# Kernel optimization log

Hardware: AMD Instinct MI355X
Metric: run time of the kernel (lower is better)

Reference implementation:

```python
import jax, jax.numpy as jnp
import numpy as np

B, T, V, E, H = 512, 256, 50000, 512, 1024


def setup_inputs() -> dict:
    key = jax.random.key(0)
    ks = jax.random.split(key, 10)
    s_in = 1.0 / np.sqrt(E + H)  # torch Linear default init scale
    s_fc = 1.0 / np.sqrt(H)
    return {
        "x": jax.random.randint(ks[0], (B, T), 0, V),
        "emb": jax.random.normal(ks[1], (V, E), dtype=jnp.float32),
        "W_r": jax.random.uniform(ks[2], (E + H, H), jnp.float32, -s_in, s_in),
        "b_r": jax.random.uniform(ks[3], (H,), jnp.float32, -s_in, s_in),
        "W_z": jax.random.uniform(ks[4], (E + H, H), jnp.float32, -s_in, s_in),
        "b_z": jax.random.uniform(ks[5], (H,), jnp.float32, -s_in, s_in),
        "W_c": jax.random.uniform(ks[6], (E + H, H), jnp.float32, -s_in, s_in),
        "b_c": jax.random.uniform(ks[7], (H,), jnp.float32, -s_in, s_in),
        "W_fc": jax.random.uniform(ks[8], (H, 1), jnp.float32, -s_fc, s_fc),
        "b_fc": jax.random.uniform(ks[9], (1,), jnp.float32, -s_fc, s_fc),
    }


def reference(x, emb, W_r, b_r, W_z, b_z, W_c, b_c, W_fc, b_fc):
    embedded = emb[x]                      # [B, T, E]
    xs = jnp.swapaxes(embedded, 0, 1)      # [T, B, E] for scan over time
    h0 = jnp.zeros((x.shape[0], H), dtype=emb.dtype)

    # fuse r and z gates: same input, one GEMM
    W_rz = jnp.concatenate([W_r, W_z], axis=1)   # [E+H, 2H]
    b_rz = jnp.concatenate([b_r, b_z], axis=0)   # [2H]

    def step(h, xt):
        combined = jnp.concatenate([xt, h], axis=1)          # [B, E+H]
        rz = jax.nn.sigmoid(combined @ W_rz + b_rz)          # [B, 2H]
        r, z = rz[:, :H], rz[:, H:]
        cc = jnp.concatenate([xt, r * h], axis=1)            # [B, E+H]
        h_tilde = jnp.tanh(cc @ W_c + b_c)                   # [B, H]
        h_new = (1.0 - z) * h + z * h_tilde
        return h_new, None

    h_T, _ = jax.lax.scan(step, h0, xs)
    return jax.nn.sigmoid(h_T @ W_fc + b_fc)                 # [B, 1]
```

## Files before the change

kernel.cpp:

```cpp
#include <hip/hip_runtime.h>
#include <hip/hip_bf16.h>

#define B_ 512
#define T_ 256
#define E_ 512
#define H_ 1024
#define K_ 1536

typedef __attribute__((ext_vector_type(4))) float f32x4;
typedef __attribute__((ext_vector_type(8))) short s16x8;
typedef __attribute__((ext_vector_type(4))) unsigned int u32x4;
typedef __attribute__((ext_vector_type(2))) unsigned int u32x2;

typedef unsigned int u32_g __attribute__((address_space(1)));
typedef unsigned int u32_l __attribute__((address_space(3)));

static __device__ __forceinline__ void gload16(const void* g, void* l) {
    __builtin_amdgcn_global_load_lds((const u32_g*)g, (u32_l*)l, 16, 0, 0);
}

static __device__ __forceinline__ short f2b(float f) {
    union { float f; unsigned u; } v; v.f = f;
    unsigned r = v.u + 0x7FFFu + ((v.u >> 16) & 1u);
    return (short)(r >> 16);
}
static __device__ __forceinline__ float bf2f(short s) {
    union { unsigned u; float f; } v; v.u = ((unsigned)(unsigned short)s) << 16;
    return v.f;
}
static __device__ __forceinline__ float sigmoidf_(float v) {
    return 1.f / (1.f + expf(-v));
}

#define WAITV(n) asm volatile("s_waitcnt vmcnt(" #n ")" ::: "memory")
#define WAITL    asm volatile("s_waitcnt lgkmcnt(0)" ::: "memory")
#define SB0 __builtin_amdgcn_sched_barrier(0)

static __device__ __forceinline__ u32x4 load16sc(const short* p) {
    u32x4 r;
    asm volatile("global_load_dwordx4 %0, %1, off sc1" : "=v"(r) : "v"(p));
    return r;
}
static __device__ __forceinline__ u32x2 load8sc(const short* p) {
    u32x2 r;
    asm volatile("global_load_dwordx2 %0, %1, off sc1" : "=v"(r) : "v"(p));
    return r;
}
static __device__ __forceinline__ void store2sc(const short* p, unsigned v) {
    asm volatile("global_store_short %0, %1, off sc1" :: "v"(p), "v"(v) : "memory");
}

#define FR(buf, row, k) \
    (*(const s16x8*)&(buf)[(row) * 128 + ((((k) >> 3) ^ ((row) & 7)) << 3)])


__global__ __launch_bounds__(256) void prep_fast(
    const float* __restrict__ W_r, const float* __restrict__ W_z,
    const float* __restrict__ W_c, const float* __restrict__ emb,
    short* __restrict__ We, short* __restrict__ Wh, short* __restrict__ embb,
    float* __restrict__ hbuf, short* __restrict__ hb16, unsigned* __restrict__ flags)
{
    const int NW = 3072 * 1536;
    const int NE = 50048 * 512;
    const int NH = 512 * 1024;
    const int NF = 8192;
    const int total = NW + NE + NH + NF;
    for (int idx = blockIdx.x * 256 + threadIdx.x; idx < total; idx += gridDim.x * 256) {
        if (idx < NW) {
            int n = idx / 1536, k = idx - n * 1536;
            const float* W = n < 1024 ? W_r : (n < 2048 ? W_z : W_c);
            float v = W[(size_t)k * 1024 + (n & 1023)];
            if (k < 512) We[(size_t)n * 512 + k] = f2b(v);
            else         Wh[(size_t)n * 1024 + (k - 512)] = f2b(v);
        } else if (idx < NW + NE) {
            int e = idx - NW; int row = e >> 9;
            embb[e] = row < 50000 ? f2b(emb[e]) : (short)0;
        } else if (idx < NW + NE + NH) {
            int h = idx - NW - NE;
            hbuf[h] = 0.f; hb16[h] = 0;
        } else {
            flags[idx - NW - NE - NH] = 0u;
        }
    }
}

__global__ __launch_bounds__(256) void vproj_gemm(
    const short* __restrict__ embb, const short* __restrict__ We,
    short* __restrict__ vp)
{
    __shared__ short As[128 * 64];
    __shared__ short Bs[128 * 64];
    const int tid = threadIdx.x, lane = tid & 63, w = tid >> 6;
    const int wm = (w >> 1) * 64, wn = (w & 1) * 64;
    const int m0 = blockIdx.x * 128, n0 = blockIdx.y * 128;
    f32x4 acc[4][4] = {};
    for (int kc = 0; kc < 8; ++kc) {
        int k0 = kc * 64;
        #pragma unroll
        for (int ii = 0; ii < 4; ++ii) {
            int i = w * 4 + ii;
            int row = i * 8 + (lane >> 3), kk = (lane & 7) * 8;
            gload16(embb + (size_t)(m0 + row) * 512 + k0 + kk, As + i * 512);
            gload16(We   + (size_t)(n0 + row) * 512 + k0 + kk, Bs + i * 512);
        }
        __syncthreads();
        #pragma unroll
        for (int kk = 0; kk < 64; kk += 32) {
            s16x8 a[4], b[4];
            #pragma unroll
            for (int f = 0; f < 4; ++f) {
                a[f] = *(const s16x8*)&As[(wm + f * 16 + (lane & 15)) * 64 + kk + (lane >> 4) * 8];
                b[f] = *(const s16x8*)&Bs[(wn + f * 16 + (lane & 15)) * 64 + kk + (lane >> 4) * 8];
            }
            #pragma unroll
            for (int fm = 0; fm < 4; ++fm)
            #pragma unroll
            for (int fn = 0; fn < 4; ++fn)
                acc[fm][fn] = __builtin_amdgcn_mfma_f32_16x16x32_bf16(a[fm], b[fn], acc[fm][fn], 0, 0, 0);
        }
        __syncthreads();
    }
    #pragma unroll
    for (int fm = 0; fm < 4; ++fm)
    #pragma unroll
    for (int fn = 0; fn < 4; ++fn)
    #pragma unroll
    for (int r = 0; r < 4; ++r) {
        int row = m0 + wm + fm * 16 + (lane >> 4) * 4 + r;
        int col = n0 + wn + fn * 16 + (lane & 15);
        vp[(size_t)row * 3072 + col] = f2b(acc[fm][fn][r]);
    }
}

static __device__ __forceinline__ void groupbar2(unsigned* gf, int member, unsigned gen) {
    WAITV(0);
    __syncthreads();
    if (threadIdx.x == 0) {
        __hip_atomic_store(&gf[member * 16], gen,
                           __ATOMIC_RELAXED, __HIP_MEMORY_SCOPE_AGENT);
    }
    if (threadIdx.x < 32) {
        int spins = 0;
        while (__hip_atomic_load(&gf[threadIdx.x * 16],
                                 __ATOMIC_RELAXED, __HIP_MEMORY_SCOPE_AGENT) < gen) {
            __builtin_amdgcn_s_sleep(1);
            if (++spins > (1 << 18)) break;
        }
    }
    __syncthreads();
}

template<int PH>
static __device__ __forceinline__ void phaseX(
    const short* __restrict__ Ab,
    const short* __restrict__ Wh,
    const short* __restrict__ vp, const int* __restrict__ xidxL,
    int g, int n, int t,
    short* AL, short* BL, short* XpL, float* zL, short* hL,
    const float* br, const float* bz, float bc,
    short* __restrict__ rh16, short* __restrict__ hb16,
    float* __restrict__ hbuf, f32x4& h_reg)
{
    const int tid = threadIdx.x, lane = tid & 63, w = tid >> 6;
    const int wm = (w >> 1) * 16;
    const int wn = (PH == 1) ? (w & 1) * 32 : (w & 1) * 16;
    constexpr int BROWS = (PH == 1) ? 64 : 32;
    constexpr int BJ    = (PH == 1) ? 4 : 2;
    constexpr int BUFSZ = BROWS * 128;

    u32x4 xp4; u32x2 xp2;
    if constexpr (PH == 1) {
        int row = tid >> 3, part = tid & 7;
        int col = (part < 4) ? (n * 32 + part * 8) : (1024 + n * 32 + (part - 4) * 8);
        xp4 = load16sc(vp + (size_t)xidxL[row] * 3072 + col);
    } else {
        int row = tid >> 3, part = tid & 7;
        xp2 = load8sc(vp + (size_t)xidxL[row] * 3072 + 2048 + n * 32 + part * 4);
    }

    auto issueA = [&](int c, u32x4* dst) {
        #pragma unroll
        for (int j = 0; j < 2; ++j) {
            int sid = j * 256 + tid, row = sid >> 4, sg = (sid & 15) ^ (row & 7);
            dst[j] = load16sc(Ab + (size_t)row * 1024 + c * 128 + sg * 8);
        }
    };
    auto issueB = [&](int c, int buf) {
        #pragma unroll
        for (int j = 0; j < BJ; ++j) {
            int sid = j * 256 + tid, row = sid >> 4, sg = (sid & 15) ^ (row & 7);
            int grow;
            if constexpr (PH == 1) grow = (row < 32) ? (n * 32 + row) : (1024 + n * 32 + row - 32);
            else                   grow = 2048 + n * 32 + row;
            gload16(Wh + (size_t)grow * 1024 + c * 128 + sg * 8,
                    BL + buf * BUFSZ + (j * 256 + w * 64) * 8);
        }
    };
    auto writeA = [&](int buf, const u32x4* src) {
        #pragma unroll
        for (int j = 0; j < 2; ++j) {
            int sid = j * 256 + tid;
            *(u32x4*)&AL[buf * 4096 + sid * 8] = src[j];
        }
    };

    u32x4 ra[2][2];
    issueA(0, ra[0]); issueB(0, 0);
    issueA(1, ra[1]); issueB(1, 1);
    if constexpr (PH == 1) { WAITV(6); } else { WAITV(4); }
    SB0;
    writeA(0, ra[0]);
    {
        int row = tid >> 3, part = tid & 7;
        if constexpr (PH == 1) {
            int dst = (part < 4) ? part * 8 : (32 + (part - 4) * 8);
            *(u32x4*)&XpL[row * 64 + dst] = xp4;
        } else {
            *(u32x2*)&XpL[row * 32 + part * 4] = xp2;
        }
    }
    WAITL;
    __builtin_amdgcn_s_barrier();
    SB0;

    f32x4 acc[2] = {};
    #pragma unroll
    for (int kc = 0; kc < 8; ++kc) {
        if (kc < 6) { issueA(kc + 2, ra[kc & 1]); issueB(kc + 2, (kc + 2) % 3); }
        const short* Ac = AL + (kc & 1) * 4096;
        const short* Bc = BL + (kc % 3) * BUFSZ;
        #pragma unroll
        for (int ks = 0; ks < 4; ++ks) {
            const int kf = ks * 32 + (lane >> 4) * 8;
            s16x8 a = FR(Ac, wm + (lane & 15), kf);
            if constexpr (PH == 1) {
                s16x8 b0 = FR(Bc, wn + (lane & 15), kf);
                s16x8 b1 = FR(Bc, wn + 16 + (lane & 15), kf);
                acc[0] = __builtin_amdgcn_mfma_f32_16x16x32_bf16(a, b0, acc[0], 0, 0, 0);
                acc[1] = __builtin_amdgcn_mfma_f32_16x16x32_bf16(a, b1, acc[1], 0, 0, 0);
            } else {
                s16x8 b0 = FR(Bc, wn + (lane & 15), kf);
                acc[0] = __builtin_amdgcn_mfma_f32_16x16x32_bf16(a, b0, acc[0], 0, 0, 0);
            }
        }
        if (kc < 7) {
            if (kc < 6) { if constexpr (PH == 1) { WAITV(6); } else { WAITV(4); } }
            else        { WAITV(0); }
            SB0;
            writeA((kc + 1) & 1, ra[(kc + 1) & 1]);
            WAITL;
            __builtin_amdgcn_s_barrier();
            SB0;
        }
    }

    const int rl0 = wm + (lane >> 4) * 4;
    if constexpr (PH == 1) {
        if ((w & 1) == 0) {
            #pragma unroll
            for (int fn = 0; fn < 2; ++fn) {
                int cl = fn * 16 + (lane & 15);
                #pragma unroll
                for (int ri = 0; ri < 4; ++ri) {
                    int rl = rl0 + ri;
                    float v = acc[fn][ri] + bf2f(XpL[rl * 64 + cl]) + br[fn];
                    float rr = sigmoidf_(v);
                    float hv = bf2f(hL[rl * 32 + cl]);
                    store2sc(rh16 + (size_t)(g * 32 + rl) * 1024 + n * 32 + cl,
                             (unsigned)(unsigned short)f2b(rr * hv));
                }
            }
        } else {
            #pragma unroll
            for (int fn = 0; fn < 2; ++fn) {
                int zc = fn * 16 + (lane & 15);
                #pragma unroll
                for (int ri = 0; ri < 4; ++ri) {
                    int rl = rl0 + ri;
                    float v = acc[fn][ri] + bf2f(XpL[rl * 64 + 32 + zc]) + bz[fn];
                    zL[rl * 32 + zc] = sigmoidf_(v);
                }
            }
        }
    } else {
        int cl2 = wn + (lane & 15);
        #pragma unroll
        for (int ri = 0; ri < 4; ++ri) {
            int rl = rl0 + ri;
            float v = acc[0][ri] + bf2f(XpL[rl * 32 + cl2]) + bc;
            float c = tanhf(v);
            float zv = zL[rl * 32 + cl2];
            float h = h_reg[ri];
            float hn = h + zv * (c - h);
            h_reg[ri] = hn;
            short hb = f2b(hn);
            store2sc(hb16 + (size_t)(g * 32 + rl) * 1024 + n * 32 + cl2,
                     (unsigned)(unsigned short)hb);
            hL[rl * 32 + cl2] = hb;
            if (t == T_ - 1)
                hbuf[(size_t)(g * 32 + rl) * 1024 + n * 32 + cl2] = hn;
        }
    }
}

__global__ __launch_bounds__(256, 2) void gru_persistent(
    const int* __restrict__ x, const short* __restrict__ Wh,
    const short* __restrict__ vp,
    const float* __restrict__ b_r, const float* __restrict__ b_z,
    const float* __restrict__ b_c,
    float* __restrict__ hbuf, short* __restrict__ hb16,
    short* __restrict__ rh16, unsigned* __restrict__ flags)
{
    __shared__ short AL[2 * 4096];
    __shared__ short BL[3 * 8192];
    __shared__ short XpL[2048];
    __shared__ float zL[1024];
    __shared__ short hL[1024];
    __shared__ int xidxL[32];

    const int bid = blockIdx.x;
    const int g = bid >> 5, n = bid & 31;
    unsigned* gf = flags + g * 512;

    const int tid = threadIdx.x, lane = tid & 63, w = tid >> 6;
    const int wm = (w >> 1) * 16, wn2 = (w & 1) * 16;

    float br[2], bz[2], bc;
    #pragma unroll
    for (int fn = 0; fn < 2; ++fn) {
        br[fn] = b_r[n * 32 + fn * 16 + (lane & 15)];
        bz[fn] = b_z[n * 32 + fn * 16 + (lane & 15)];
    }
    bc = b_c[n * 32 + wn2 + (lane & 15)];

    f32x4 h_reg = {0.f, 0.f, 0.f, 0.f};
    #pragma unroll
    for (int ri = 0; ri < 4; ++ri)
        hL[(wm + (lane >> 4) * 4 + ri) * 32 + wn2 + (lane & 15)] = 0;

    for (int t = 0; t < T_; ++t) {
        if (tid < 32) xidxL[tid] = x[(g * 32 + tid) * T_ + t];
        __syncthreads();
        phaseX<1>(hb16 + (size_t)(g * 32) * 1024, Wh, vp, xidxL, g, n, t,
                  AL, BL, XpL, zL, hL, br, bz, bc, rh16, hb16, hbuf, h_reg);
        groupbar2(gf, n, 2 * t + 1);
        phaseX<2>(rh16 + (size_t)(g * 32) * 1024, Wh, vp, xidxL, g, n, t,
                  AL, BL, XpL, zL, hL, br, bz, bc, rh16, hb16, hbuf, h_reg);
        if (t < T_ - 1) groupbar2(gf, n, 2 * t + 2);
    }
}

__global__ __launch_bounds__(256) void fc_kernel(
    const float* __restrict__ h, const float* __restrict__ Wfc,
    const float* __restrict__ bfc, float* __restrict__ out)
{
    int gw   = (blockIdx.x * 256 + threadIdx.x) >> 6;
    int lane = threadIdx.x & 63;
    if (gw >= B_) return;
    float s = 0.f;
    for (int j = lane; j < H_; j += 64) s += h[(size_t)gw * H_ + j] * Wfc[j];
    #pragma unroll
    for (int off = 32; off; off >>= 1) s += __shfl_down(s, off);
    if (lane == 0) out[gw] = sigmoidf_(s + bfc[0]);
}

__global__ __launch_bounds__(256) void prep_fb(
    const float* __restrict__ W_r, const float* __restrict__ W_z,
    const float* __restrict__ W_c,
    short* __restrict__ Wt_rz, short* __restrict__ Wt_c,
    float* __restrict__ hbuf, short* __restrict__ hbf16)
{
    const int PER = H_ * K_;
    int idx = blockIdx.x * 256 + threadIdx.x;
    if (idx < PER * 3) {
        int mm = idx / PER, rem = idx - mm * PER;
        int n = rem / K_, k = rem - n * K_;
        if (mm == 0)      Wt_rz[(size_t)n * K_ + k]        = f2b(W_r[(size_t)k * H_ + n]);
        else if (mm == 1) Wt_rz[(size_t)(H_ + n) * K_ + k] = f2b(W_z[(size_t)k * H_ + n]);
        else              Wt_c[(size_t)n * K_ + k]         = f2b(W_c[(size_t)k * H_ + n]);
    }
    if (idx < B_ * H_) { hbuf[idx] = 0.f; hbf16[idx] = 0; }
}

template<int MODE>
__global__ __launch_bounds__(256) void gru_gemm(
    const int* __restrict__ x, const float* __restrict__ emb,
    const short* __restrict__ Wt, const short* __restrict__ hpart,
    const float* __restrict__ bias0, const float* __restrict__ bias1,
    const float* __restrict__ hbuf, float* __restrict__ zbuf,
    short* __restrict__ rh_out, float* __restrict__ h_out,
    short* __restrict__ hb_out, int t)
{
    __shared__ short As2[64][72];
    __shared__ short Bs2[64][72];
    __shared__ int xidx2[64];
    const int tid = threadIdx.x;
    const int bm = blockIdx.x, bn = blockIdx.y;
    if (tid < 64) xidx2[tid] = x[(bm * 64 + tid) * T_ + t];
    f32x4 acc[2][2] = {};
    const int m  = tid >> 2;
    const int ks = (tid & 3) * 16;
    const int w  = tid >> 6, lane = tid & 63;
    const int wm = (w >> 1) * 32, wn = (w & 1) * 32;
    const int lr = lane & 15, lk = (lane >> 4) * 8;
    __syncthreads();
    for (int kt = 0; kt < 24; ++kt) {
        const int k0 = kt * 64;
        if (k0 < E_) {
            const int row = xidx2[m];
            const float4* src = (const float4*)&emb[(size_t)row * E_ + k0 + ks];
            short tmp[16];
            #pragma unroll
            for (int v = 0; v < 4; ++v) {
                float4 f = src[v];
                tmp[v*4+0] = f2b(f.x); tmp[v*4+1] = f2b(f.y);
                tmp[v*4+2] = f2b(f.z); tmp[v*4+3] = f2b(f.w);
            }
            *(s16x8*)&As2[m][ks]     = *(const s16x8*)&tmp[0];
            *(s16x8*)&As2[m][ks + 8] = *(const s16x8*)&tmp[8];
        } else {
            const s16x8* src = (const s16x8*)&hpart[(size_t)(bm*64 + m) * H_ + (k0 - E_ + ks)];
            *(s16x8*)&As2[m][ks]     = src[0];
            *(s16x8*)&As2[m][ks + 8] = src[1];
        }
        {
            const s16x8* src = (const s16x8*)&Wt[(size_t)(bn*64 + m) * K_ + k0 + ks];
            *(s16x8*)&Bs2[m][ks]     = src[0];
            *(s16x8*)&Bs2[m][ks + 8] = src[1];
        }
        __syncthreads();
        #pragma unroll
        for (int kk = 0; kk < 64; kk += 32) {
            s16x8 a0 = *(const s16x8*)&As2[wm      + lr][kk + lk];
            s16x8 a1 = *(const s16x8*)&As2[wm + 16 + lr][kk + lk];
            s16x8 b0 = *(const s16x8*)&Bs2[wn      + lr][kk + lk];
            s16x8 b1 = *(const s16x8*)&Bs2[wn + 16 + lr][kk + lk];
            acc[0][0] = __builtin_amdgcn_mfma_f32_16x16x32_bf16(a0, b0, acc[0][0], 0, 0, 0);
            acc[0][1] = __builtin_amdgcn_mfma_f32_16x16x32_bf16(a0, b1, acc[0][1], 0, 0, 0);
            acc[1][0] = __builtin_amdgcn_mfma_f32_16x16x32_bf16(a1, b0, acc[1][0], 0, 0, 0);
            acc[1][1] = __builtin_amdgcn_mfma_f32_16x16x32_bf16(a1, b1, acc[1][1], 0, 0, 0);
        }
        __syncthreads();
    }
    #pragma unroll
    for (int fm = 0; fm < 2; ++fm)
    #pragma unroll
    for (int fn = 0; fn < 2; ++fn)
    #pragma unroll
    for (int r = 0; r < 4; ++r) {
        const int row = bm * 64 + wm + fm * 16 + ((lane >> 4) * 4 + r);
        const int n   = bn * 64 + wn + fn * 16 + (lane & 15);
        float v = acc[fm][fn][r];
        if (MODE == 0) {
            if (n < H_) {
                float rr = sigmoidf_(v + bias0[n]);
                size_t idx = (size_t)row * H_ + n;
                rh_out[idx] = f2b(rr * hbuf[idx]);
            } else {
                int nz = n - H_;
                zbuf[(size_t)row * H_ + nz] = sigmoidf_(v + bias1[nz]);
            }
        } else {
            float ht = tanhf(v + bias0[n]);
            size_t idx = (size_t)row * H_ + n;
            float h = hbuf[idx], z = zbuf[idx];
            float hn = (1.f - z) * h + z * ht;
            h_out[idx]  = hn;
            hb_out[idx] = f2b(hn);
        }
    }
}

extern "C" void kernel_launch(void* const* d_in, const int* in_sizes, int n_in,
                              void* d_out, int out_size, void* d_ws, size_t ws_size,
                              hipStream_t stream) {
    const int*   x    = (const int*)  d_in[0];
    const float* emb  = (const float*)d_in[1];
    const float* W_r  = (const float*)d_in[2];
    const float* b_r  = (const float*)d_in[3];
    const float* W_z  = (const float*)d_in[4];
    const float* b_z  = (const float*)d_in[5];
    const float* W_c  = (const float*)d_in[6];
    const float* b_c  = (const float*)d_in[7];
    const float* W_fc = (const float*)d_in[8];
    const float* b_fc = (const float*)d_in[9];

    char* ws = (char*)d_ws;
    const size_t NEED = 374489088ULL;

    if (ws_size >= NEED) {
        short*    We    = (short*)(ws);
        short*    Wh    = (short*)(ws + 3145728);
        short*    embb  = (short*)(ws + 9437184);
        short*    vp    = (short*)(ws + 60686336);
        float*    hbuf  = (float*)(ws + 368181248);
        short*    hb16  = (short*)(ws + 370278400);
        short*    rh16  = (short*)(ws + 371326976);
        unsigned* flags = (unsigned*)(ws + 372375552);

        prep_fast<<<2048, 256, 0, stream>>>(W_r, W_z, W_c, emb, We, Wh, embb, hbuf, hb16, flags);
        vproj_gemm<<<dim3(391, 24), 256, 0, stream>>>(embb, We, vp);
        gru_persistent<<<512, 256, 0, stream>>>(x, Wh, vp, b_r, b_z, b_c,
                                                hbuf, hb16, rh16, flags);
        fc_kernel<<<128, 256, 0, stream>>>(hbuf, W_fc, b_fc, (float*)d_out);
    } else {
        short* Wt_rz  = (short*)(ws);
        short* Wt_c   = (short*)(ws + 6291456);
        float* hbuf   = (float*)(ws + 9437184);
        short* hbf16  = (short*)(ws + 11534336);
        short* rhbf16 = (short*)(ws + 12582912);
        float* zbuf   = (float*)(ws + 13631488);

        prep_fb<<<18432, 256, 0, stream>>>(W_r, W_z, W_c, Wt_rz, Wt_c, hbuf, hbf16);
        for (int t = 0; t < T_; ++t) {
            gru_gemm<0><<<dim3(8, 32), 256, 0, stream>>>(
                x, emb, Wt_rz, hbf16, b_r, b_z, hbuf, zbuf, rhbf16, nullptr, nullptr, t);
            gru_gemm<1><<<dim3(8, 16), 256, 0, stream>>>(
                x, emb, Wt_c, rhbf16, b_c, nullptr, hbuf, zbuf, nullptr, hbuf, hbf16, t);
        }
        fc_kernel<<<128, 256, 0, stream>>>(hbuf, W_fc, b_fc, (float*)d_out);
    }
}
```

Baseline: 5.459 ms.

## Halve GRU persistent block to two waves using 32x32x16 MFMA tiles

```diff
diff --git a/kernel.cpp b/kernel.cpp
--- a/kernel.cpp
+++ b/kernel.cpp
@@ -8,9 +8,9 @@
 #define K_ 1536
 
 typedef __attribute__((ext_vector_type(4))) float f32x4;
+typedef __attribute__((ext_vector_type(16))) float f32x16;
 typedef __attribute__((ext_vector_type(8))) short s16x8;
 typedef __attribute__((ext_vector_type(4))) unsigned int u32x4;
-typedef __attribute__((ext_vector_type(2))) unsigned int u32x2;
 
 typedef unsigned int u32_g __attribute__((address_space(1)));
 typedef unsigned int u32_l __attribute__((address_space(3)));
@@ -39,11 +39,6 @@
 static __device__ __forceinline__ u32x4 load16sc(const short* p) {
     u32x4 r;
     asm volatile("global_load_dwordx4 %0, %1, off sc1" : "=v"(r) : "v"(p));
-    return r;
-}
-static __device__ __forceinline__ u32x2 load8sc(const short* p) {
-    u32x2 r;
-    asm volatile("global_load_dwordx2 %0, %1, off sc1" : "=v"(r) : "v"(p));
     return r;
 }
 static __device__ __forceinline__ void store2sc(const short* p, unsigned v) {
@@ -152,99 +147,106 @@
 
 template<int PH>
 static __device__ __forceinline__ void phaseX(
-    const short* __restrict__ Ab,
-    const short* __restrict__ Wh,
+    const short* __restrict__ Ab, const short* __restrict__ Wh,
     const short* __restrict__ vp, const int* __restrict__ xidxL,
     int g, int n, int t,
     short* AL, short* BL, short* XpL, float* zL, short* hL,
-    const float* br, const float* bz, float bc,
+    float br, float bz, float bc,
     short* __restrict__ rh16, short* __restrict__ hb16,
-    float* __restrict__ hbuf, f32x4& h_reg)
+    float* __restrict__ hbuf, f32x4* h_reg)
 {
     const int tid = threadIdx.x, lane = tid & 63, w = tid >> 6;
-    const int wm = (w >> 1) * 16;
-    const int wn = (PH == 1) ? (w & 1) * 32 : (w & 1) * 16;
-    constexpr int BROWS = (PH == 1) ? 64 : 32;
-    constexpr int BJ    = (PH == 1) ? 4 : 2;
-    constexpr int BUFSZ = BROWS * 128;
-
-    u32x4 xp4; u32x2 xp2;
+    constexpr int BJ = (PH == 1) ? 8 : 4;
+
+    u32x4 xpr[2];
     if constexpr (PH == 1) {
-        int row = tid >> 3, part = tid & 7;
-        int col = (part < 4) ? (n * 32 + part * 8) : (1024 + n * 32 + (part - 4) * 8);
-        xp4 = load16sc(vp + (size_t)xidxL[row] * 3072 + col);
+        #pragma unroll
+        for (int j = 0; j < 2; ++j) {
+            int sid = j * 128 + tid, row = sid >> 3, part = sid & 7;
+            int col = (part < 4) ? (n * 32 + part * 8) : (1024 + n * 32 + (part - 4) * 8);
+            xpr[j] = load16sc(vp + (size_t)xidxL[row] * 3072 + col);
+        }
     } else {
-        int row = tid >> 3, part = tid & 7;
-        xp2 = load8sc(vp + (size_t)xidxL[row] * 3072 + 2048 + n * 32 + part * 4);
+        int row = tid >> 2, part = tid & 3;
+        xpr[0] = load16sc(vp + (size_t)xidxL[row] * 3072 + 2048 + n * 32 + part * 8);
     }
 
     auto issueA = [&](int c, u32x4* dst) {
         #pragma unroll
-        for (int j = 0; j < 2; ++j) {
-            int sid = j * 256 + tid, row = sid >> 4, sg = (sid & 15) ^ (row & 7);
+        for (int j = 0; j < 4; ++j) {
+            int sid = j * 128 + tid, row = sid >> 4, sg = (sid & 15) ^ (row & 7);
             dst[j] = load16sc(Ab + (size_t)row * 1024 + c * 128 + sg * 8);
+        }
+    };
+    auto writeA = [&](int buf, const u32x4* src) {
+        #pragma unroll
+        for (int j = 0; j < 4; ++j) {
+            int sid = j * 128 + tid;
+            *(u32x4*)&AL[buf * 4096 + sid * 8] = src[j];
         }
     };
     auto issueB = [&](int c, int buf) {
         #pragma unroll
         for (int j = 0; j < BJ; ++j) {
-            int sid = j * 256 + tid, row = sid >> 4, sg = (sid & 15) ^ (row & 7);
+            int sid = j * 128 + w * 64 + lane;
+            int row = sid >> 4, sg = (sid & 15) ^ (row & 7);
             int grow;
             if constexpr (PH == 1) grow = (row < 32) ? (n * 32 + row) : (1024 + n * 32 + row - 32);
             else                   grow = 2048 + n * 32 + row;
             gload16(Wh + (size_t)grow * 1024 + c * 128 + sg * 8,
-                    BL + buf * BUFSZ + (j * 256 + w * 64) * 8);
+                    BL + buf * 8192 + (j * 128 + w * 64) * 8);
         }
     };
-    auto writeA = [&](int buf, const u32x4* src) {
-        #pragma unroll
-        for (int j = 0; j < 2; ++j) {
-            int sid = j * 256 + tid;
-            *(u32x4*)&AL[buf * 4096 + sid * 8] = src[j];
-        }
-    };
-
-    u32x4 ra[2][2];
+
+    u32x4 ra[2][4];
     issueA(0, ra[0]); issueB(0, 0);
     issueA(1, ra[1]); issueB(1, 1);
-    if constexpr (PH == 1) { WAITV(6); } else { WAITV(4); }
+    if constexpr (PH == 1) { WAITV(12); } else { WAITV(8); }
     SB0;
     writeA(0, ra[0]);
-    {
-        int row = tid >> 3, part = tid & 7;
-        if constexpr (PH == 1) {
+    if constexpr (PH == 1) {
+        #pragma unroll
+        for (int j = 0; j < 2; ++j) {
+            int sid = j * 128 + tid, row = sid >> 3, part = sid & 7;
             int dst = (part < 4) ? part * 8 : (32 + (part - 4) * 8);
-            *(u32x4*)&XpL[row * 64 + dst] = xp4;
-        } else {
-            *(u32x2*)&XpL[row * 32 + part * 4] = xp2;
-        }
+            *(u32x4*)&XpL[row * 64 + dst] = xpr[j];
+        }
+    } else {
+        int row = tid >> 2, part = tid & 3;
+        *(u32x4*)&XpL[row * 32 + part * 8] = xpr[0];
     }
     WAITL;
     __builtin_amdgcn_s_barrier();
     SB0;
 
-    f32x4 acc[2] = {};
+    f32x16 acc1 = {};
+    f32x4  acc2[2] = {};
     #pragma unroll
     for (int kc = 0; kc < 8; ++kc) {
         if (kc < 6) { issueA(kc + 2, ra[kc & 1]); issueB(kc + 2, (kc + 2) % 3); }
         const short* Ac = AL + (kc & 1) * 4096;
-        const short* Bc = BL + (kc % 3) * BUFSZ;
-        #pragma unroll
-        for (int ks = 0; ks < 4; ++ks) {
-            const int kf = ks * 32 + (lane >> 4) * 8;
-            s16x8 a = FR(Ac, wm + (lane & 15), kf);
-            if constexpr (PH == 1) {
-                s16x8 b0 = FR(Bc, wn + (lane & 15), kf);
-                s16x8 b1 = FR(Bc, wn + 16 + (lane & 15), kf);
-                acc[0] = __builtin_amdgcn_mfma_f32_16x16x32_bf16(a, b0, acc[0], 0, 0, 0);
-                acc[1] = __builtin_amdgcn_mfma_f32_16x16x32_bf16(a, b1, acc[1], 0, 0, 0);
-            } else {
-                s16x8 b0 = FR(Bc, wn + (lane & 15), kf);
-                acc[0] = __builtin_amdgcn_mfma_f32_16x16x32_bf16(a, b0, acc[0], 0, 0, 0);
+        const short* Bc = BL + (kc % 3) * 8192;
+        if constexpr (PH == 1) {
+            #pragma unroll
+            for (int ks = 0; ks < 8; ++ks) {
+                const int kf = ks * 16 + (lane >> 5) * 8;
+                s16x8 a = FR(Ac, (lane & 31), kf);
+                s16x8 b = FR(Bc, w * 32 + (lane & 31), kf);
+                acc1 = __builtin_amdgcn_mfma_f32_32x32x16_bf16(a, b, acc1, 0, 0, 0);
+            }
+        } else {
+            #pragma unroll
+            for (int ks = 0; ks < 4; ++ks) {
+                const int kf = ks * 32 + (lane >> 4) * 8;
+                s16x8 a0 = FR(Ac, (lane & 15), kf);
+                s16x8 a1 = FR(Ac, 16 + (lane & 15), kf);
+                s16x8 b  = FR(Bc, w * 16 + (lane & 15), kf);
+                acc2[0] = __builtin_amdgcn_mfma_f32_16x16x32_bf16(a0, b, acc2[0], 0, 0, 0);
+                acc2[1] = __builtin_amdgcn_mfma_f32_16x16x32_bf16(a1, b, acc2[1], 0, 0, 0);
             }
         }
         if (kc < 7) {
-            if (kc < 6) { if constexpr (PH == 1) { WAITV(6); } else { WAITV(4); } }
+            if (kc < 6) { if constexpr (PH == 1) { WAITV(12); } else { WAITV(8); } }
             else        { WAITV(0); }
             SB0;
             writeA((kc + 1) & 1, ra[(kc + 1) & 1]);
@@ -254,56 +256,50 @@
         }
     }
 
-    const int rl0 = wm + (lane >> 4) * 4;
     if constexpr (PH == 1) {
-        if ((w & 1) == 0) {
-            #pragma unroll
-            for (int fn = 0; fn < 2; ++fn) {
-                int cl = fn * 16 + (lane & 15);
-                #pragma unroll
-                for (int ri = 0; ri < 4; ++ri) {
-                    int rl = rl0 + ri;
-                    float v = acc[fn][ri] + bf2f(XpL[rl * 64 + cl]) + br[fn];
-                    float rr = sigmoidf_(v);
-                    float hv = bf2f(hL[rl * 32 + cl]);
-                    store2sc(rh16 + (size_t)(g * 32 + rl) * 1024 + n * 32 + cl,
-                             (unsigned)(unsigned short)f2b(rr * hv));
-                }
+        const int col = lane & 31;
+        if (w == 0) {
+            #pragma unroll
+            for (int reg = 0; reg < 16; ++reg) {
+                int row = (reg & 3) + 8 * (reg >> 2) + 4 * (lane >> 5);
+                float v = acc1[reg] + bf2f(XpL[row * 64 + col]) + br;
+                float rr = sigmoidf_(v);
+                float hv = bf2f(hL[row * 32 + col]);
+                store2sc(rh16 + (size_t)(g * 32 + row) * 1024 + n * 32 + col,
+                         (unsigned)(unsigned short)f2b(rr * hv));
             }
         } else {
             #pragma unroll
-            for (int fn = 0; fn < 2; ++fn) {
-                int zc = fn * 16 + (lane & 15);
-                #pragma unroll
-                for (int ri = 0; ri < 4; ++ri) {
-                    int rl = rl0 + ri;
-                    float v = acc[fn][ri] + bf2f(XpL[rl * 64 + 32 + zc]) + bz[fn];
-                    zL[rl * 32 + zc] = sigmoidf_(v);
-                }
+            for (int reg = 0; reg < 16; ++reg) {
+                int row = (reg & 3) + 8 * (reg >> 2) + 4 * (lane >> 5);
+                float v = acc1[reg] + bf2f(XpL[row * 64 + 32 + col]) + bz;
+                zL[row * 32 + col] = sigmoidf_(v);
             }
         }
     } else {
-        int cl2 = wn + (lane & 15);
+        const int col = w * 16 + (lane & 15);
+        #pragma unroll
+        for (int fm = 0; fm < 2; ++fm)
         #pragma unroll
         for (int ri = 0; ri < 4; ++ri) {
-            int rl = rl0 + ri;
-            float v = acc[0][ri] + bf2f(XpL[rl * 32 + cl2]) + bc;
+            int row = fm * 16 + (lane >> 4) * 4 + ri;
+            float v = acc2[fm][ri] + bf2f(XpL[row * 32 + col]) + bc;
             float c = tanhf(v);
-            float zv = zL[rl * 32 + cl2];
-            float h = h_reg[ri];
+            float zv = zL[row * 32 + col];
+            float h = h_reg[fm][ri];
             float hn = h + zv * (c - h);
-            h_reg[ri] = hn;
+            h_reg[fm][ri] = hn;
             short hb = f2b(hn);
-            store2sc(hb16 + (size_t)(g * 32 + rl) * 1024 + n * 32 + cl2,
+            store2sc(hb16 + (size_t)(g * 32 + row) * 1024 + n * 32 + col,
                      (unsigned)(unsigned short)hb);
-            hL[rl * 32 + cl2] = hb;
+            hL[row * 32 + col] = hb;
             if (t == T_ - 1)
-                hbuf[(size_t)(g * 32 + rl) * 1024 + n * 32 + cl2] = hn;
-        }
-    }
-}
-
-__global__ __launch_bounds__(256, 2) void gru_persistent(
+                hbuf[(size_t)(g * 32 + row) * 1024 + n * 32 + col] = hn;
+        }
+    }
+}
+
+__global__ __launch_bounds__(128) void gru_persistent(
     const int* __restrict__ x, const short* __restrict__ Wh,
     const short* __restrict__ vp,
     const float* __restrict__ b_r, const float* __restrict__ b_z,
@@ -323,20 +319,16 @@
     unsigned* gf = flags + g * 512;
 
     const int tid = threadIdx.x, lane = tid & 63, w = tid >> 6;
-    const int wm = (w >> 1) * 16, wn2 = (w & 1) * 16;
-
-    float br[2], bz[2], bc;
-    #pragma unroll
-    for (int fn = 0; fn < 2; ++fn) {
-        br[fn] = b_r[n * 32 + fn * 16 + (lane & 15)];
-        bz[fn] = b_z[n * 32 + fn * 16 + (lane & 15)];
-    }
-    bc = b_c[n * 32 + wn2 + (lane & 15)];
-
-    f32x4 h_reg = {0.f, 0.f, 0.f, 0.f};
-    #pragma unroll
-    for (int ri = 0; ri < 4; ++ri)
-        hL[(wm + (lane >> 4) * 4 + ri) * 32 + wn2 + (lane & 15)] = 0;
+
+    float br = b_r[n * 32 + (lane & 31)];
+    float bz = b_z[n * 32 + (lane & 31)];
+    float bc = b_c[n * 32 + w * 16 + (lane & 15)];
+
+    f32x4 h_reg[2] = {};
+    {
+        s16x8 zf = {};
+        *(s16x8*)&hL[tid * 8] = zf;
+    }
 
     for (int t = 0; t < T_; ++t) {
         if (tid < 32) xidxL[tid] = x[(g * 32 + tid) * T_ + t];
@@ -500,7 +492,7 @@
 
         prep_fast<<<2048, 256, 0, stream>>>(W_r, W_z, W_c, emb, We, Wh, embb, hbuf, hb16, flags);
         vproj_gemm<<<dim3(391, 24), 256, 0, stream>>>(embb, We, vp);
-        gru_persistent<<<512, 256, 0, stream>>>(x, Wh, vp, b_r, b_z, b_c,
+        gru_persistent<<<512, 128, 0, stream>>>(x, Wh, vp, b_r, b_z, b_c,
                                                 hbuf, hb16, rh16, flags);
         fc_kernel<<<128, 256, 0, stream>>>(hbuf, W_fc, b_fc, (float*)d_out);
     } else {
```

Measured after the change: 6.151 ms. 12.7% more time.

## Prefetch next phase weights and embeddings across group barriers, deepen A pipeline

Applied to the files above, without the earlier changes.

```diff
diff --git a/kernel.cpp b/kernel.cpp
--- a/kernel.cpp
+++ b/kernel.cpp
@@ -132,125 +132,135 @@
     }
 }
 
-static __device__ __forceinline__ void groupbar2(unsigned* gf, int member, unsigned gen) {
-    WAITV(0);
-    __syncthreads();
-    if (threadIdx.x == 0) {
+static __device__ __forceinline__ void barrier_fs(unsigned* gf, int member, unsigned gen) {
+    __builtin_amdgcn_s_barrier();
+    if (threadIdx.x == 0)
         __hip_atomic_store(&gf[member * 16], gen,
                            __ATOMIC_RELAXED, __HIP_MEMORY_SCOPE_AGENT);
-    }
-    if (threadIdx.x < 32) {
+    if ((threadIdx.x & 63) < 32) {
         int spins = 0;
-        while (__hip_atomic_load(&gf[threadIdx.x * 16],
+        while (__hip_atomic_load(&gf[(threadIdx.x & 31) * 16],
                                  __ATOMIC_RELAXED, __HIP_MEMORY_SCOPE_AGENT) < gen) {
             __builtin_amdgcn_s_sleep(1);
             if (++spins > (1 << 18)) break;
         }
     }
-    __syncthreads();
-}
-
+    __builtin_amdgcn_s_barrier();
+}
+
+static __device__ __forceinline__ void issueA2(const short* Ab, int c, u32x4* dst) {
+    const int tid = threadIdx.x;
+    #pragma unroll
+    for (int j = 0; j < 2; ++j) {
+        int sid = j * 256 + tid, row = sid >> 4, sg = (sid & 15) ^ (row & 7);
+        dst[j] = load16sc(Ab + (size_t)row * 1024 + c * 128 + sg * 8);
+    }
+}
+static __device__ __forceinline__ void writeA2(short* AL, int buf, const u32x4* src) {
+    const int tid = threadIdx.x;
+    #pragma unroll
+    for (int j = 0; j < 2; ++j) {
+        int sid = j * 256 + tid;
+        *(u32x4*)&AL[buf * 4096 + sid * 8] = src[j];
+    }
+}
 template<int PH>
-static __device__ __forceinline__ void phaseX(
-    const short* __restrict__ Ab,
-    const short* __restrict__ Wh,
-    const short* __restrict__ vp, const int* __restrict__ xidxL,
+static __device__ __forceinline__ void issueB(const short* Wh, short* BL, int n, int c, int buf) {
+    const int tid = threadIdx.x, lane = tid & 63, w = tid >> 6;
+    constexpr int BJ    = (PH == 1) ? 4 : 2;
+    constexpr int BUFSZ = (PH == 1) ? 8192 : 4096;
+    #pragma unroll
+    for (int j = 0; j < BJ; ++j) {
+        int sid = j * 256 + tid, row = sid >> 4, sg = (sid & 15) ^ (row & 7);
+        int grow;
+        if constexpr (PH == 1) grow = (row < 32) ? (n * 32 + row) : (1024 + n * 32 + row - 32);
+        else                   grow = 2048 + n * 32 + row;
+        gload16(Wh + (size_t)grow * 1024 + c * 128 + sg * 8,
+                BL + buf * BUFSZ + (j * 256 + w * 64) * 8);
+    }
+}
+template<int PH>
+static __device__ __forceinline__ u32x4 gather_xp(const short* vp, int xv, int n) {
+    const int part = threadIdx.x & 7;
+    u32x4 r = {};
+    if constexpr (PH == 1) {
+        int col = (part < 4) ? (n * 32 + part * 8) : (1024 + n * 32 + (part - 4) * 8);
+        r = load16sc(vp + (size_t)xv * 3072 + col);
+    } else {
+        u32x2 t2 = load8sc(vp + (size_t)xv * 3072 + 2048 + n * 32 + part * 4);
+        r.x = t2.x; r.y = t2.y;
+    }
+    return r;
+}
+
+template<int PH>
+static __device__ __forceinline__ void phase_run(
+    const short* __restrict__ Ab, const short* __restrict__ Wh,
     int g, int n, int t,
     short* AL, short* BL, short* XpL, float* zL, short* hL,
-    const float* br, const float* bz, float bc,
+    const float* br, const float* bz, float bc, u32x4 xp,
     short* __restrict__ rh16, short* __restrict__ hb16,
     float* __restrict__ hbuf, f32x4& h_reg)
 {
     const int tid = threadIdx.x, lane = tid & 63, w = tid >> 6;
     const int wm = (w >> 1) * 16;
     const int wn = (PH == 1) ? (w & 1) * 32 : (w & 1) * 16;
-    constexpr int BROWS = (PH == 1) ? 64 : 32;
-    constexpr int BJ    = (PH == 1) ? 4 : 2;
-    constexpr int BUFSZ = BROWS * 128;
-
-    u32x4 xp4; u32x2 xp2;
-    if constexpr (PH == 1) {
-        int row = tid >> 3, part = tid & 7;
-        int col = (part < 4) ? (n * 32 + part * 8) : (1024 + n * 32 + (part - 4) * 8);
-        xp4 = load16sc(vp + (size_t)xidxL[row] * 3072 + col);
-    } else {
-        int row = tid >> 3, part = tid & 7;
-        xp2 = load8sc(vp + (size_t)xidxL[row] * 3072 + 2048 + n * 32 + part * 4);
-    }
-
-    auto issueA = [&](int c, u32x4* dst) {
-        #pragma unroll
-        for (int j = 0; j < 2; ++j) {
-            int sid = j * 256 + tid, row = sid >> 4, sg = (sid & 15) ^ (row & 7);
-            dst[j] = load16sc(Ab + (size_t)row * 1024 + c * 128 + sg * 8);
-        }
-    };
-    auto issueB = [&](int c, int buf) {
-        #pragma unroll
-        for (int j = 0; j < BJ; ++j) {
-            int sid = j * 256 + tid, row = sid >> 4, sg = (sid & 15) ^ (row & 7);
-            int grow;
-            if constexpr (PH == 1) grow = (row < 32) ? (n * 32 + row) : (1024 + n * 32 + row - 32);
-            else                   grow = 2048 + n * 32 + row;
-            gload16(Wh + (size_t)grow * 1024 + c * 128 + sg * 8,
-                    BL + buf * BUFSZ + (j * 256 + w * 64) * 8);
-        }
-    };
-    auto writeA = [&](int buf, const u32x4* src) {
-        #pragma unroll
-        for (int j = 0; j < 2; ++j) {
-            int sid = j * 256 + tid;
-            *(u32x4*)&AL[buf * 4096 + sid * 8] = src[j];
-        }
-    };
-
-    u32x4 ra[2][2];
-    issueA(0, ra[0]); issueB(0, 0);
-    issueA(1, ra[1]); issueB(1, 1);
-    if constexpr (PH == 1) { WAITV(6); } else { WAITV(4); }
-    SB0;
-    writeA(0, ra[0]);
+    constexpr int BUFSZ = (PH == 1) ? 8192 : 4096;
+
+    u32x4 ra[4][2];
+    issueA2(Ab, 0, ra[0]); issueA2(Ab, 1, ra[1]);
+    issueA2(Ab, 2, ra[2]); issueA2(Ab, 3, ra[3]);
+    WAITV(6); SB0;
+    writeA2(AL, 0, ra[0]);
     {
         int row = tid >> 3, part = tid & 7;
         if constexpr (PH == 1) {
             int dst = (part < 4) ? part * 8 : (32 + (part - 4) * 8);
-            *(u32x4*)&XpL[row * 64 + dst] = xp4;
+            *(u32x4*)&XpL[row * 64 + dst] = xp;
         } else {
-            *(u32x2*)&XpL[row * 32 + part * 4] = xp2;
+            u32x2 v2; v2.x = xp.x; v2.y = xp.y;
+            *(u32x2*)&XpL[row * 32 + part * 4] = v2;
         }
     }
     WAITL;
     __builtin_amdgcn_s_barrier();
     SB0;
 
-    f32x4 acc[2] = {};
+    f32x4 acc0 = {}, acc1 = {};
     #pragma unroll
     for (int kc = 0; kc < 8; ++kc) {
-        if (kc < 6) { issueA(kc + 2, ra[kc & 1]); issueB(kc + 2, (kc + 2) % 3); }
+        if (kc < 4) issueA2(Ab, kc + 4, ra[kc & 3]);
+        if (kc < 6) issueB<PH>(Wh, BL, n, kc + 2, (kc + 2) % 3);
+        SB0;
         const short* Ac = AL + (kc & 1) * 4096;
         const short* Bc = BL + (kc % 3) * BUFSZ;
         #pragma unroll
         for (int ks = 0; ks < 4; ++ks) {
             const int kf = ks * 32 + (lane >> 4) * 8;
-            s16x8 a = FR(Ac, wm + (lane & 15), kf);
+            s16x8 a  = FR(Ac, wm + (lane & 15), kf);
+            s16x8 b0 = FR(Bc, wn + (lane & 15), kf);
+            acc0 = __builtin_amdgcn_mfma_f32_16x16x32_bf16(a, b0, acc0, 0, 0, 0);
             if constexpr (PH == 1) {
-                s16x8 b0 = FR(Bc, wn + (lane & 15), kf);
                 s16x8 b1 = FR(Bc, wn + 16 + (lane & 15), kf);
-                acc[0] = __builtin_amdgcn_mfma_f32_16x16x32_bf16(a, b0, acc[0], 0, 0, 0);
-                acc[1] = __builtin_amdgcn_mfma_f32_16x16x32_bf16(a, b1, acc[1], 0, 0, 0);
+                acc1 = __builtin_amdgcn_mfma_f32_16x16x32_bf16(a, b1, acc1, 0, 0, 0);
+            }
+        }
+        if (kc < 7) {
+            if constexpr (PH == 1) {
+                if (kc == 0) { WAITV(10); } else if (kc <= 3) { WAITV(6); }
+                else if (kc <= 5) { WAITV(4); } else { WAITV(0); }
             } else {
-                s16x8 b0 = FR(Bc, wn + (lane & 15), kf);
-                acc[0] = __builtin_amdgcn_mfma_f32_16x16x32_bf16(a, b0, acc[0], 0, 0, 0);
-            }
-        }
-        if (kc < 7) {
-            if (kc < 6) { if constexpr (PH == 1) { WAITV(6); } else { WAITV(4); } }
-            else        { WAITV(0); }
+                if (kc == 0) { WAITV(8); } else if (kc <= 3) { WAITV(4); }
+                else if (kc <= 5) { WAITV(2); } else { WAITV(0); }
+            }
             SB0;
-            writeA((kc + 1) & 1, ra[(kc + 1) & 1]);
+            writeA2(AL, (kc + 1) & 1, ra[(kc + 1) & 3]);
             WAITL;
             __builtin_amdgcn_s_barrier();
             SB0;
+        } else {
+            SB0;
+            __builtin_amdgcn_s_barrier();
         }
     }
 
@@ -263,7 +273,7 @@
                 #pragma unroll
                 for (int ri = 0; ri < 4; ++ri) {
                     int rl = rl0 + ri;
-                    float v = acc[fn][ri] + bf2f(XpL[rl * 64 + cl]) + br[fn];
+                    float v = (fn ? acc1[ri] : acc0[ri]) + bf2f(XpL[rl * 64 + cl]) + br[fn];
                     float rr = sigmoidf_(v);
                     float hv = bf2f(hL[rl * 32 + cl]);
                     store2sc(rh16 + (size_t)(g * 32 + rl) * 1024 + n * 32 + cl,
@@ -277,28 +287,28 @@
                 #pragma unroll
                 for (int ri = 0; ri < 4; ++ri) {
                     int rl = rl0 + ri;
-                    float v = acc[fn][ri] + bf2f(XpL[rl * 64 + 32 + zc]) + bz[fn];
+                    float v = (fn ? acc1[ri] : acc0[ri]) + bf2f(XpL[rl * 64 + 32 + zc]) + bz[fn];
                     zL[rl * 32 + zc] = sigmoidf_(v);
                 }
             }
         }
     } else {
-        int cl2 = wn + (lane & 15);
+        const int cl = wn + (lane & 15);
         #pragma unroll
         for (int ri = 0; ri < 4; ++ri) {
             int rl = rl0 + ri;
-            float v = acc[0][ri] + bf2f(XpL[rl * 32 + cl2]) + bc;
+            float v = acc0[ri] + bf2f(XpL[rl * 32 + cl]) + bc;
             float c = tanhf(v);
-            float zv = zL[rl * 32 + cl2];
+            float zv = zL[rl * 32 + cl];
             float h = h_reg[ri];
             float hn = h + zv * (c - h);
             h_reg[ri] = hn;
             short hb = f2b(hn);
-            store2sc(hb16 + (size_t)(g * 32 + rl) * 1024 + n * 32 + cl2,
+            store2sc(hb16 + (size_t)(g * 32 + rl) * 1024 + n * 32 + cl,
                      (unsigned)(unsigned short)hb);
-            hL[rl * 32 + cl2] = hb;
+            hL[rl * 32 + cl] = hb;
             if (t == T_ - 1)
-                hbuf[(size_t)(g * 32 + rl) * 1024 + n * 32 + cl2] = hn;
+                hbuf[(size_t)(g * 32 + rl) * 1024 + n * 32 + cl] = hn;
         }
     }
 }
@@ -316,37 +326,56 @@
     __shared__ short XpL[2048];
     __shared__ float zL[1024];
     __shared__ short hL[1024];
-    __shared__ int xidxL[32];
 
     const int bid = blockIdx.x;
     const int g = bid >> 5, n = bid & 31;
     unsigned* gf = flags + g * 512;
-
     const int tid = threadIdx.x, lane = tid & 63, w = tid >> 6;
-    const int wm = (w >> 1) * 16, wn2 = (w & 1) * 16;
-
-    float br[2], bz[2], bc;
+
+    float br[2], bz[2];
     #pragma unroll
     for (int fn = 0; fn < 2; ++fn) {
         br[fn] = b_r[n * 32 + fn * 16 + (lane & 15)];
         bz[fn] = b_z[n * 32 + fn * 16 + (lane & 15)];
     }
-    bc = b_c[n * 32 + wn2 + (lane & 15)];
+    const float bc = b_c[n * 32 + (w & 1) * 16 + (lane & 15)];
 
     f32x4 h_reg = {0.f, 0.f, 0.f, 0.f};
-    #pragma unroll
-    for (int ri = 0; ri < 4; ++ri)
-        hL[(wm + (lane >> 4) * 4 + ri) * 32 + wn2 + (lane & 15)] = 0;
+    ((u32x2*)hL)[tid] = (u32x2){0u, 0u};
+
+    const short* Ab1 = hb16 + (size_t)(g * 32) * 1024;
+    const short* Ab2 = rh16 + (size_t)(g * 32) * 1024;
+
+    int xv = x[(g * 32 + (tid >> 3)) * T_ + 0];
+    SB0;
+    u32x4 xp = gather_xp<1>(vp, xv, n);
+    issueB<1>(Wh, BL, n, 0, 0);
+    issueB<1>(Wh, BL, n, 1, 1);
+    SB0;
 
     for (int t = 0; t < T_; ++t) {
-        if (tid < 32) xidxL[tid] = x[(g * 32 + tid) * T_ + t];
-        __syncthreads();
-        phaseX<1>(hb16 + (size_t)(g * 32) * 1024, Wh, vp, xidxL, g, n, t,
-                  AL, BL, XpL, zL, hL, br, bz, bc, rh16, hb16, hbuf, h_reg);
-        groupbar2(gf, n, 2 * t + 1);
-        phaseX<2>(rh16 + (size_t)(g * 32) * 1024, Wh, vp, xidxL, g, n, t,
-                  AL, BL, XpL, zL, hL, br, bz, bc, rh16, hb16, hbuf, h_reg);
-        if (t < T_ - 1) groupbar2(gf, n, 2 * t + 2);
+        phase_run<1>(Ab1, Wh, g, n, t, AL, BL, XpL, zL, hL,
+                     br, bz, bc, xp, rh16, hb16, hbuf, h_reg);
+        u32x4 xp2 = gather_xp<2>(vp, xv, n);
+        issueB<2>(Wh, BL, n, 0, 0);
+        issueB<2>(Wh, BL, n, 1, 1);
+        WAITV(5);
+        WAITL;
+        SB0;
+        barrier_fs(gf, n, 2 * t + 1);
+
+        int xv_next = x[(g * 32 + (tid >> 3)) * T_ + ((t < T_ - 1) ? t + 1 : t)];
+        SB0;
+        phase_run<2>(Ab2, Wh, g, n, t, AL, BL, XpL, zL, hL,
+                     br, bz, bc, xp2, rh16, hb16, hbuf, h_reg);
+        xv = xv_next;
+        xp = gather_xp<1>(vp, xv, n);
+        issueB<1>(Wh, BL, n, 0, 0);
+        issueB<1>(Wh, BL, n, 1, 1);
+        WAITV(9);
+        WAITL;
+        SB0;
+        if (t < T_ - 1) barrier_fs(gf, n, 2 * t + 2);
     }
 }
 
```

Result: slower. 5.999 ms (+9.9%).
